# Kernel optimization log

Measured on AMD Instinct MI355X. Metric: run time of the kernel, lower is better.

The kernel has to match this reference:

```python
import jax, jax.numpy as jnp
import numpy as np

B, CIN, COUT = 4, 256, 256
H, W = 48, 48
KH = KW = 7
SH = SW = 1
PH = PW = 3
REL = COUT // 2  # rel_size with groups=1


def setup_inputs() -> dict:
    key = jax.random.key(0)
    ks = jax.random.split(key, 7)
    fan = float(CIN)
    x = jax.random.normal(ks[0], (B, CIN, H, W), jnp.float32)
    w_q = jax.random.normal(ks[1], (COUT, CIN), jnp.float32) * (2.0 / fan) ** 0.5
    w_k = jax.random.normal(ks[2], (COUT, CIN), jnp.float32) * (2.0 / fan) ** 0.5
    w_v = jax.random.normal(ks[3], (COUT, CIN), jnp.float32) * (2.0 / fan) ** 0.5
    bound = 1.0 / np.sqrt(COUT)
    bias = jax.random.uniform(ks[4], (1, COUT, 1, 1), jnp.float32, -bound, bound)
    rel_x = jax.random.normal(ks[5], (REL, KW), jnp.float32)
    rel_y = jax.random.normal(ks[6], (COUT - REL, KH), jnp.float32)
    return {"x": x, "w_q": w_q, "w_k": w_k, "w_v": w_v, "bias": bias,
            "rel_x": rel_x, "rel_y": rel_y}


def reference(x, w_q, w_k, w_v, bias, rel_x, rel_y):
    b = x.shape[0]
    ph, pw = H + 2 * PH, W + 2 * PW
    fh = (ph - KH) // SH + 1
    fw = (pw - KW) // SW + 1
    xp = jnp.pad(x, ((0, 0), (0, 0), (PH, PH), (PW, PW)))
    # 1x1 convs (groups=1) as channel matmuls
    vq = jnp.einsum('oc,bchw->bohw', w_q, xp)
    vk = jnp.einsum('oc,bchw->bohw', w_k, xp)
    vv = jnp.einsum('oc,bchw->bohw', w_v, xp)
    # query at window centers: [b, C, fh, fw]
    win_q = vq[:, :, (KH - 1) // 2: ph - KH // 2: SH, (KW - 1) // 2: pw - KW // 2: SW]
    # relative position terms (sum over channel halves)
    qx = jnp.einsum('bxhw,xk->bhwk', win_q[:, :REL], rel_x)        # [b,fh,fw,kw]
    qy = jnp.einsum('byhw,yk->bhwk', win_q[:, REL:], rel_y)        # [b,fh,fw,kh]
    # overlapping windows via gather (equivalent to torch unfold)
    I = jnp.arange(fh)[:, None] * SH + jnp.arange(KH)[None, :]     # [fh,kh]
    J = jnp.arange(fw)[:, None] * SW + jnp.arange(KW)[None, :]     # [fw,kw]
    win_k = vk[:, :, I[:, None, :, None], J[None, :, None, :]]     # [b,C,fh,fw,kh,kw]
    # channel-summed attention logits (shared across channels, as in source)
    scores = jnp.einsum('bchw,bchwkl->bhwkl', win_q, win_k)
    scores = scores + qy[:, :, :, :, None] + qx[:, :, :, None, :]
    attn = jax.nn.softmax(scores.reshape(b, fh, fw, KH * KW), axis=-1)
    attn = attn.reshape(b, fh, fw, KH, KW)
    win_v = vv[:, :, I[:, None, :, None], J[None, :, None, :]]     # [b,C,fh,fw,kh,kw]
    out = jnp.einsum('bhwkl,bchwkl->bchw', attn, win_v) + bias
    return out
```

## Files before the change

### kernel.cpp

```cpp
#include <hip/hip_runtime.h>

#define BB 4
#define CC 256
#define HH 48
#define WW 48
#define HWHW 2304
#define KK 49
#define RELN 128

#define QSZ (BB*CC*HWHW)
#define ATTNOFF (3*QSZ)
#define SBUF_FLOATS (BB*HH*64*WW)
#define WTOFF (ATTNOFF + SBUF_FLOATS)
#define WT_FLOATS 196608
#define KBOFF (WTOFF + WT_FLOATS)
#define KB_FLOATS 3145728
#define RBOFF (KBOFF + KB_FLOATS)

typedef short bf16x8 __attribute__((ext_vector_type(8)));
typedef float f32x4 __attribute__((ext_vector_type(4)));

__device__ __forceinline__ void split_bf16(float f, unsigned short& hi, unsigned short& lo)
{
    unsigned u = __float_as_uint(f);
    hi = (unsigned short)(u >> 16);
    float r = f - __uint_as_float(u & 0xFFFF0000u);
    unsigned v = __float_as_uint(r);
    v += 0x7FFFu + ((v >> 16) & 1u);
    lo = (unsigned short)(v >> 16);
}

__device__ __forceinline__ void gload16(const uint4* g, uint4* l)
{
    __builtin_amdgcn_global_load_lds(
        (const __attribute__((address_space(1))) void*)g,
        (__attribute__((address_space(3))) void*)l, 16, 0, 0);
}

__global__ __launch_bounds__(256) void prep_kernel(
    const float* __restrict__ x,
    const float* __restrict__ wq, const float* __restrict__ wk,
    const float* __restrict__ wvp,
    const float* __restrict__ relx, const float* __restrict__ rely,
    unsigned short* __restrict__ xt, unsigned short* __restrict__ wt,
    float* __restrict__ ws)
{
    __shared__ unsigned short lds[32*520];
    const int bid = blockIdx.x;
    const int t = threadIdx.x;

    if (bid < 288) {
        const int b = bid / 72;
        const int hw0 = (bid % 72) * 32;
        const int hw = t & 31, cp = t >> 5;
        #pragma unroll 4
        for (int i = 0; i < 32; ++i) {
            int c = i*8 + cp;
            float f = x[((size_t)b*CC + c)*HWHW + hw0 + hw];
            unsigned short hi, lo; split_bf16(f, hi, lo);
            int ch = i*2;
            lds[hw*520 + ((ch       ^ (hw&7))*8) + cp] = hi;
            lds[hw*520 + (((ch + 1) ^ (hw&7))*8) + cp] = lo;
        }
        __syncthreads();
        const int hw2 = t >> 3, u = t & 7;
        uint4* xt4 = (uint4*)xt;
        const size_t rowbase = ((size_t)b*HWHW + hw0 + hw2) * 64;
        #pragma unroll
        for (int j = 0; j < 8; ++j) {
            int chunk = j*8 + u;
            uint4 v = *(const uint4*)&lds[hw2*520 + chunk*8];
            xt4[rowbase + chunk] = v;
        }
        return;
    }
    if (bid < 384) {
        const int tt = (bid - 288)*256 + t;
        const int m = tt >> 5, kg = tt & 31;
        const float* src = (m < 256) ? wq : (m < 512) ? wk : wvp;
        const float* row = src + (size_t)(m & 255)*256 + kg*8;
        unsigned short h[8], l[8];
        #pragma unroll
        for (int j = 0; j < 8; ++j) split_bf16(row[j], h[j], l[j]);
        uint4 hv, lv;
        hv.x = (unsigned)h[0] | ((unsigned)h[1]<<16); hv.y = (unsigned)h[2] | ((unsigned)h[3]<<16);
        hv.z = (unsigned)h[4] | ((unsigned)h[5]<<16); hv.w = (unsigned)h[6] | ((unsigned)h[7]<<16);
        lv.x = (unsigned)l[0] | ((unsigned)l[1]<<16); lv.y = (unsigned)l[2] | ((unsigned)l[3]<<16);
        lv.z = (unsigned)l[4] | ((unsigned)l[5]<<16); lv.w = (unsigned)l[6] | ((unsigned)l[7]<<16);
        uint4* dstrow = (uint4*)wt + (size_t)m*64;
        const int ks = kg >> 2, s_hi = 2*(kg & 3);
        dstrow[ks*8 + ( s_hi      ^ (m&7))] = hv;
        dstrow[ks*8 + ((s_hi + 1) ^ (m&7))] = lv;
        return;
    }
    if (bid < 576) {
        uint4* kb4 = (uint4*)(ws + KBOFF);
        const uint4 z = make_uint4(0u,0u,0u,0u);
        int u0 = (bid - 384)*256 + t;
        #pragma unroll
        for (int it = 0; it < 4; ++it) {
            int u = u0 + it*49152;
            int bch = u >> 7, rem = u & 127;
            int r16 = rem >> 3, gr = rem & 7;
            int r = (r16 < 3) ? r16 : 48 + r16;
            kb4[((size_t)bch*64 + r)*8 + gr] = z;
        }
        return;
    }
    {
        unsigned short* rb = (unsigned short*)(ws + RBOFF);
        #pragma unroll
        for (int it = 0; it < 4; ++it) {
            int idx = t + it*256;
            int gi  = idx & 7;
            int l   = (idx >> 3) & 15;
            int ck4 = (idx >> 7) & 3;
            int rel = idx >> 9;
            int isLo = gi >> 2, g4i = gi & 3;
            unsigned short vals[8];
            #pragma unroll
            for (int j = 0; j < 8; ++j) {
                int cl = ck4*32 + g4i*8 + j;
                float f = (l < 7) ? (rel ? rely[cl*7 + l] : relx[cl*7 + l]) : 0.f;
                unsigned short hi, lo; split_bf16(f, hi, lo);
                vals[j] = isLo ? lo : hi;
            }
            int slot = gi ^ (l & 7);
            unsigned short* dst = rb + (((size_t)rel*4 + ck4)*16 + l)*64 + slot*8;
            uint4 pack;
            pack.x = (unsigned)vals[0] | ((unsigned)vals[1]<<16);
            pack.y = (unsigned)vals[2] | ((unsigned)vals[3]<<16);
            pack.z = (unsigned)vals[4] | ((unsigned)vals[5]<<16);
            pack.w = (unsigned)vals[6] | ((unsigned)vals[7]<<16);
            *(uint4*)dst = pack;
        }
    }
}

__global__ __launch_bounds__(256) void proj_gemm_kernel(
    const unsigned short* __restrict__ xt,
    const unsigned short* __restrict__ wt,
    float* __restrict__ ws)
{
    __shared__ uint4 smem[2][1024];
    const int n0 = blockIdx.x * 64;
    const int m0 = blockIdx.y * 64;
    const int b = n0 / HWHW;
    const int hwb = n0 % HWHW;
    const int tid = threadIdx.x;
    const int wid = tid >> 6, ln = tid & 63;
    const int wm = wid >> 1, wn = wid & 1;
    const int l15 = ln & 15, g = ln >> 4;

    f32x4 acc[2][2];
    #pragma unroll
    for (int i = 0; i < 2; ++i)
        #pragma unroll
        for (int j = 0; j < 2; ++j) acc[i][j] = (f32x4){0.f,0.f,0.f,0.f};

    const uint4* wt4 = (const uint4*)wt;
    const uint4* xt4 = (const uint4*)xt;
    const int lrow = ln >> 3, lslot = ln & 7;

    #define STAGE(bf, ks)                                                          \
        {                                                                          \
            _Pragma("unroll")                                                      \
            for (int i = 0; i < 2; ++i) {                                          \
                int seg = wid*2 + i;                                               \
                int row = seg*8 + lrow;                                            \
                gload16(wt4 + (size_t)(m0 + row)*64 + (ks)*8 + lslot,              \
                        &smem[bf][seg*64]);                                        \
                gload16(xt4 + (size_t)(n0 + row)*64 + (ks)*8 + lslot,              \
                        &smem[bf][512 + seg*64]);                                  \
            }                                                                      \
        }

    STAGE(0, 0);
    #pragma unroll
    for (int ks = 0; ks < 8; ++ks) {
        const int cur = ks & 1;
        if (ks < 7) STAGE(cur ^ 1, ks + 1);
        if (ks < 7) asm volatile("s_waitcnt vmcnt(4)" ::: "memory");
        else        asm volatile("s_waitcnt vmcnt(0)" ::: "memory");
        __builtin_amdgcn_s_barrier();
        __builtin_amdgcn_sched_barrier(0);
        bf16x8 aH[2], aL[2], bH[2], bL[2];
        #pragma unroll
        for (int mt = 0; mt < 2; ++mt) {
            int rA = wm*32 + mt*16 + l15;
            aH[mt] = *(const bf16x8*)&smem[cur][rA*8 + ((2*g)   ^ (rA&7))];
            aL[mt] = *(const bf16x8*)&smem[cur][rA*8 + ((2*g+1) ^ (rA&7))];
        }
        #pragma unroll
        for (int nt = 0; nt < 2; ++nt) {
            int rB = wn*32 + nt*16 + l15;
            bH[nt] = *(const bf16x8*)&smem[cur][512 + rB*8 + ((2*g)   ^ (rB&7))];
            bL[nt] = *(const bf16x8*)&smem[cur][512 + rB*8 + ((2*g+1) ^ (rB&7))];
        }
        #pragma unroll
        for (int mt = 0; mt < 2; ++mt)
            #pragma unroll
            for (int nt = 0; nt < 2; ++nt) {
                acc[mt][nt] = __builtin_amdgcn_mfma_f32_16x16x32_bf16(aH[mt], bH[nt], acc[mt][nt], 0, 0, 0);
                acc[mt][nt] = __builtin_amdgcn_mfma_f32_16x16x32_bf16(aH[mt], bL[nt], acc[mt][nt], 0, 0, 0);
                acc[mt][nt] = __builtin_amdgcn_mfma_f32_16x16x32_bf16(aL[mt], bH[nt], acc[mt][nt], 0, 0, 0);
            }
        if (ks < 7) {
            asm volatile("s_waitcnt lgkmcnt(0)" ::: "memory");
            __builtin_amdgcn_s_barrier();
        }
    }
    #undef STAGE

    const int proj = m0 >> 8;
    if (proj == 2) {
        #pragma unroll
        for (int mt = 0; mt < 2; ++mt) {
            int chb = (m0 & 255) + wm*32 + mt*16 + 4*g;
            int ch4 = chb >> 2;
            #pragma unroll
            for (int nt = 0; nt < 2; ++nt) {
                int hw = hwb + wn*32 + nt*16 + l15;
                float* dst = ws + (size_t)2*QSZ + (((size_t)b*64 + ch4)*HWHW + hw)*4;
                *(f32x4*)dst = acc[mt][nt];
            }
        }
        return;
    }
    __syncthreads();
    unsigned short* eb = (unsigned short*)&smem[0][0];
    #pragma unroll
    for (int mt = 0; mt < 2; ++mt) {
        const int chb = (m0 & 255) + wm*32 + mt*16 + 4*g;
        const int ckl = (chb >> 5) & 1;
        const int p = chb & 31, g8 = p >> 3, half = (p >> 2) & 1;
        #pragma unroll
        for (int nt = 0; nt < 2; ++nt) {
            const int hwl = wn*32 + nt*16 + l15;
            const int w = (hwb + hwl) % 48;
            const int key = (proj == 0 ? w : w + 3) & 7;
            f32x4 v = acc[mt][nt];
            unsigned short h0,h1,h2,h3,q0,q1,q2,q3;
            split_bf16(v[0],h0,q0); split_bf16(v[1],h1,q1);
            split_bf16(v[2],h2,q2); split_bf16(v[3],h3,q3);
            uint2 hv, lv;
            hv.x = (unsigned)h0 | ((unsigned)h1<<16); hv.y = (unsigned)h2 | ((unsigned)h3<<16);
            lv.x = (unsigned)q0 | ((unsigned)q1<<16); lv.y = (unsigned)q2 | ((unsigned)q3<<16);
            const int base = (ckl*64 + hwl)*64;
            *(uint2*)(eb + base + ((g8 ^ key)*8 + half*4))     = hv;
            *(uint2*)(eb + base + (((g8+4) ^ key)*8 + half*4)) = lv;
        }
    }
    __syncthreads();
    const int ck0 = (m0 & 255) >> 5;
    if (proj == 0) {
        const uint4* src = (const uint4*)eb;
        uint4* qb4 = (uint4*)ws;
        #pragma unroll
        for (int ckl2 = 0; ckl2 < 2; ++ckl2) {
            uint4* dst = qb4 + (((size_t)b*8 + ck0 + ckl2)*HWHW + hwb)*8;
            #pragma unroll
            for (int it = 0; it < 2; ++it)
                dst[tid + it*256] = src[ckl2*512 + tid + it*256];
        }
    } else {
        uint4* kb4 = (uint4*)(ws + KBOFF);
        const uint4* src = (const uint4*)eb;
        #pragma unroll
        for (int it = 0; it < 4; ++it) {
            int u = tid + it*256;
            int row = u >> 3, gr = u & 7;
            int ckl2 = row >> 6, hwl2 = row & 63;
            int hw2 = hwb + hwl2, h2 = hw2/48, w2 = hw2%48;
            uint4* dst = kb4 + ((((size_t)b*8 + ck0 + ckl2)*48 + h2)*64 + (w2+3))*8;
            dst[gr] = src[u];
        }
    }
}

__global__ __launch_bounds__(512) void scores2_kernel(float* __restrict__ ws)
{
    __shared__ unsigned short sAll[4096*8];
    __shared__ float sc[63][48];

    unsigned short* sQ = sAll;
    unsigned short* sK = sAll + 384*8;
    unsigned short* sR = sAll + 3968*8;

    const int bid = blockIdx.x;
    const int b = bid / 48, h = bid % 48;
    const int tid = threadIdx.x;
    const int wv = tid >> 6, ln = tid & 63;
    const int l15 = ln & 15, g4 = ln >> 4;
    const int key = l15 & 7;

    const unsigned short* QB = (const unsigned short*)ws;
    const unsigned short* KB = (const unsigned short*)(ws + KBOFF);
    const unsigned short* RB = (const unsigned short*)(ws + RBOFF);

    for (int u = tid; u < 63*48; u += 512) ((float*)sc)[u] = 0.f;

    const int dk = wv;
    const int hp = h + dk - 3;
    const bool dok = (wv < 7) && (hp >= 0) && (hp < 48);

    f32x4 acc[6], qx[3], qy[3];
    #pragma unroll
    for (int i = 0; i < 6; ++i) acc[i] = (f32x4){0.f,0.f,0.f,0.f};
    #pragma unroll
    for (int i = 0; i < 3; ++i) { qx[i] = (f32x4){0.f,0.f,0.f,0.f}; qy[i] = (f32x4){0.f,0.f,0.f,0.f}; }

    for (int ck = 0; ck < 8; ++ck) {
        #pragma unroll
        for (int e = 0; e < 8; ++e) {
            const int I = wv*8 + e;
            uint4* dst = (uint4*)sAll + I*64;
            if (I < 6) {
                int unit = I*64 + ln; int row = unit >> 3, gr = unit & 7;
                const uint4* src = (const uint4*)QB
                    + ((((size_t)b*8 + ck)*48 + h)*48 + row)*8 + gr;
                gload16(src, dst);
            } else if (I < 62) {
                int uk = (I-6)*64 + ln;
                int kri = uk >> 9;
                int wi = uk & 511; int row = wi >> 3, gr = wi & 7;
                int kh = h + kri - 3;
                if (kh >= 0 && kh < 48) {
                    const uint4* src = (const uint4*)KB
                        + ((((size_t)b*8 + ck)*48 + kh)*64 + row)*8 + gr;
                    gload16(src, dst);
                }
            } else {
                int ur = (I-62)*64 + ln; int row = ur >> 3, gr = ur & 7;
                int rel = ck >> 2, c4 = ck & 3;
                const uint4* src = (const uint4*)RB
                    + (((size_t)rel*4 + c4)*16 + row)*8 + gr;
                gload16(src, dst);
            }
        }
        __syncthreads();

        bf16x8 AH[3], AL[3];
        #pragma unroll
        for (int i = 0; i < 3; ++i) {
            const unsigned short* qr = sQ + (16*i + l15)*64;
            AH[i] = *(const bf16x8*)(qr + ((g4       ^ key)*8));
            AL[i] = *(const bf16x8*)(qr + (((g4 + 4) ^ key)*8));
        }

        if (wv < 7) {
            if (dok) {
                const unsigned short* kbase = sK + dk*4096;
                bf16x8 BH[4], BL[4];
                #pragma unroll
                for (int j = 0; j < 4; ++j) {
                    const unsigned short* kr = kbase + (j*16 + l15)*64;
                    BH[j] = *(const bf16x8*)(kr + ((g4       ^ key)*8));
                    BL[j] = *(const bf16x8*)(kr + (((g4 + 4) ^ key)*8));
                }
                #pragma unroll
                for (int i = 0; i < 3; ++i) {
                    acc[i*2]   = __builtin_amdgcn_mfma_f32_16x16x32_bf16(AH[i], BH[i],   acc[i*2],   0,0,0);
                    acc[i*2]   = __builtin_amdgcn_mfma_f32_16x16x32_bf16(AH[i], BL[i],   acc[i*2],   0,0,0);
                    acc[i*2]   = __builtin_amdgcn_mfma_f32_16x16x32_bf16(AL[i], BH[i],   acc[i*2],   0,0,0);
                    acc[i*2+1] = __builtin_amdgcn_mfma_f32_16x16x32_bf16(AH[i], BH[i+1], acc[i*2+1], 0,0,0);
                    acc[i*2+1] = __builtin_amdgcn_mfma_f32_16x16x32_bf16(AH[i], BL[i+1], acc[i*2+1], 0,0,0);
                    acc[i*2+1] = __builtin_amdgcn_mfma_f32_16x16x32_bf16(AL[i], BH[i+1], acc[i*2+1], 0,0,0);
                }
            }
        } else {
            const unsigned short* rr = sR + l15*64;
            bf16x8 RH = *(const bf16x8*)(rr + ((g4       ^ key)*8));
            bf16x8 RL = *(const bf16x8*)(rr + (((g4 + 4) ^ key)*8));
            if (ck < 4) {
                #pragma unroll
                for (int i = 0; i < 3; ++i) {
                    qx[i] = __builtin_amdgcn_mfma_f32_16x16x32_bf16(AH[i], RH, qx[i], 0,0,0);
                    qx[i] = __builtin_amdgcn_mfma_f32_16x16x32_bf16(AH[i], RL, qx[i], 0,0,0);
                    qx[i] = __builtin_amdgcn_mfma_f32_16x16x32_bf16(AL[i], RH, qx[i], 0,0,0);
                }
            } else {
                #pragma unroll
                for (int i = 0; i < 3; ++i) {
                    qy[i] = __builtin_amdgcn_mfma_f32_16x16x32_bf16(AH[i], RH, qy[i], 0,0,0);
                    qy[i] = __builtin_amdgcn_mfma_f32_16x16x32_bf16(AH[i], RL, qy[i], 0,0,0);
                    qy[i] = __builtin_amdgcn_mfma_f32_16x16x32_bf16(AL[i], RH, qy[i], 0,0,0);
                }
            }
        }
        __syncthreads();
    }

    const int n = l15;
    if (wv < 7) {
        if (dok) {
            #pragma unroll
            for (int i = 0; i < 3; ++i)
                #pragma unroll
                for (int a = 0; a < 2; ++a) {
                    f32x4 A = acc[i*2+a];
                    #pragma unroll
                    for (int r = 0; r < 4; ++r) {
                        int m = 4*g4 + r;
                        int dl = n - m + a*16;
                        if (dl >= 0 && dl < 7)
                            sc[dk*7 + dl][16*i + m] = A[r];
                    }
                }
        }
    } else {
        if (n < 7) {
            #pragma unroll
            for (int i = 0; i < 3; ++i)
                #pragma unroll
                for (int r = 0; r < 4; ++r) {
                    sc[49 + n][16*i + 4*g4 + r] = qx[i][r];
                    sc[56 + n][16*i + 4*g4 + r] = qy[i][r];
                }
        }
    }
    __syncthreads();

    if (tid < 48) {
        const int w = tid;
        float tot[KK], rx[7], ry[7];
        #pragma unroll
        for (int i = 0; i < KK; ++i) tot[i] = sc[i][w];
        #pragma unroll
        for (int l = 0; l < 7; ++l) { rx[l] = sc[49+l][w]; ry[l] = sc[56+l][w]; }
        float mx = -1e30f;
        #pragma unroll
        for (int dk2 = 0; dk2 < 7; ++dk2)
            #pragma unroll
            for (int dl = 0; dl < 7; ++dl) {
                tot[dk2*7+dl] += ry[dk2] + rx[dl];
                mx = fmaxf(mx, tot[dk2*7+dl]);
            }
        float sum = 0.f;
        #pragma unroll
        for (int i = 0; i < KK; ++i) { float e = __expf(tot[i]-mx); tot[i]=e; sum += e; }
        float inv = 1.f/sum;
        float* base = ws + ATTNOFF + ((size_t)(b*HH + h)*64)*WW + w;
        #pragma unroll
        for (int i = 0; i < KK; ++i) base[(size_t)i*WW] = tot[i]*inv;
    }
}

__global__ __launch_bounds__(128) void pv_kernel(
    const float* __restrict__ bias,
    const float* __restrict__ ws,
    float* __restrict__ out)
{
    const float* vbuf = ws + (size_t)2*QSZ;
    const float* attn = ws + ATTNOFF;

    const int bid = blockIdx.x;
    const int pxt = bid % 18;
    const int pgq = (bid / 18) % 16;
    const int b   = bid / (18*16);

    const int tid = threadIdx.x;
    const int pxg = tid & 31;
    const int pg  = pgq*4 + (tid >> 5);

    const int hw0 = pxt*128 + pxg*4;
    const int w0 = hw0 % WW;
    const int h0 = hw0 / WW;

    const float* vb = vbuf + ((size_t)b*64 + pg)*HWHW*4;
    const float* ab = attn + ((size_t)(b*HH + h0)*64)*WW;

    const float4 b4 = *(const float4*)(bias + pg*4);
    f32x4 bias4 = (f32x4){b4.x, b4.y, b4.z, b4.w};
    f32x4 acc[4];
    #pragma unroll
    for (int p = 0; p < 4; ++p) acc[p] = bias4;

    #pragma unroll
    for (int dk = 0; dk < 7; ++dk) {
        const int gr = h0 + dk - 3;
        const bool rok = (gr >= 0 && gr < HH);
        f32x4 vrow[10];
        #pragma unroll
        for (int jj = 0; jj < 10; ++jj) {
            const int gc = w0 - 3 + jj;
            vrow[jj] = (rok && gc >= 0 && gc < WW)
                ? *(const f32x4*)(vb + ((size_t)gr*WW + gc)*4)
                : (f32x4){0.f,0.f,0.f,0.f};
        }
        const float* arow = ab + (size_t)(dk*7)*WW + w0;
        #pragma unroll
        for (int dl = 0; dl < 7; ++dl) {
            const float4 av = *(const float4*)(arow + (size_t)dl*WW);
            acc[0] += vrow[dl+0] * av.x;
            acc[1] += vrow[dl+1] * av.y;
            acc[2] += vrow[dl+2] * av.z;
            acc[3] += vrow[dl+3] * av.w;
        }
    }
    #pragma unroll
    for (int c = 0; c < 4; ++c) {
        float4 o;
        o.x = acc[0][c]; o.y = acc[1][c]; o.z = acc[2][c]; o.w = acc[3][c];
        *(float4*)(out + ((size_t)b*CC + pg*4 + c)*HWHW + hw0) = o;
    }
}

extern "C" void kernel_launch(void* const* d_in, const int* in_sizes, int n_in,
                              void* d_out, int out_size, void* d_ws, size_t ws_size,
                              hipStream_t stream) {
    const float* x    = (const float*)d_in[0];
    const float* wq   = (const float*)d_in[1];
    const float* wk   = (const float*)d_in[2];
    const float* wv   = (const float*)d_in[3];
    const float* bias = (const float*)d_in[4];
    const float* relx = (const float*)d_in[5];
    const float* rely = (const float*)d_in[6];
    float* ws  = (float*)d_ws;
    float* out = (float*)d_out;
    unsigned short* xt = (unsigned short*)d_out;
    unsigned short* wt = (unsigned short*)(ws + WTOFF);

    prep_kernel<<<dim3(577), dim3(256), 0, stream>>>(x, wq, wk, wv, relx, rely, xt, wt, ws);
    proj_gemm_kernel<<<dim3(144, 12), dim3(256), 0, stream>>>(xt, wt, ws);
    scores2_kernel<<<dim3(BB*HH), dim3(512), 0, stream>>>(ws);
    pv_kernel<<<dim3(BB*16*18), dim3(128), 0, stream>>>(bias, ws, out);
}
```

Measured before the change: 74.91 us.

## Split scores kernel over channel chunks and add a separate reduce-softmax kernel

The scores kernel now splits the 8 channel chunks across 4 blocks per (batch,row), so the grid grows from 192 to 768 blocks. Each block writes its partial score and relative-position sums to workspace. A new reduce_softmax kernel adds the four partials and runs the softmax. The aim is to fill more of the 256 CUs, at the cost of one extra launch, extra global traffic for the partials, and the Q tile being reloaded in every split.

```diff
diff --git a/kernel.cpp b/kernel.cpp
--- a/kernel.cpp
+++ b/kernel.cpp
@@ -16,6 +16,7 @@
 #define KBOFF (WTOFF + WT_FLOATS)
 #define KB_FLOATS 3145728
 #define RBOFF (KBOFF + KB_FLOATS)
+#define PARTOFF (RBOFF + 4096)
 
 typedef short bf16x8 __attribute__((ext_vector_type(8)));
 typedef float f32x4 __attribute__((ext_vector_type(4)));
@@ -288,7 +289,9 @@
     unsigned short* sR = sAll + 3968*8;
 
     const int bid = blockIdx.x;
-    const int b = bid / 48, h = bid % 48;
+    const int ckp = bid & 3;
+    const int h = (bid >> 2) % 48;
+    const int b = bid / 192;
     const int tid = threadIdx.x;
     const int wv = tid >> 6, ln = tid & 63;
     const int l15 = ln & 15, g4 = ln >> 4;
@@ -310,7 +313,8 @@
     #pragma unroll
     for (int i = 0; i < 3; ++i) { qx[i] = (f32x4){0.f,0.f,0.f,0.f}; qy[i] = (f32x4){0.f,0.f,0.f,0.f}; }
 
-    for (int ck = 0; ck < 8; ++ck) {
+    for (int cki = 0; cki < 2; ++cki) {
+        const int ck = ckp*2 + cki;
         #pragma unroll
         for (int e = 0; e < 8; ++e) {
             const int I = wv*8 + e;
@@ -421,13 +425,33 @@
     }
     __syncthreads();
 
-    if (tid < 48) {
-        const int w = tid;
+    float* pdst = ws + PARTOFF + ((size_t)(b*HH + h)*4 + ckp)*3024;
+    for (int u = tid; u < 3024; u += 512) pdst[u] = ((const float*)sc)[u];
+}
+
+__global__ __launch_bounds__(256) void reduce_softmax_kernel(float* __restrict__ ws)
+{
+    __shared__ float red[63][48];
+    const int bh = blockIdx.x;
+    const int t = threadIdx.x;
+    const float* pb = ws + PARTOFF + (size_t)bh*4*3024;
+
+    for (int u = t; u < 756; u += 256) {
+        f32x4 a = *(const f32x4*)(pb + u*4)
+                + *(const f32x4*)(pb + 3024 + u*4)
+                + *(const f32x4*)(pb + 2*3024 + u*4)
+                + *(const f32x4*)(pb + 3*3024 + u*4);
+        *(f32x4*)&((float*)red)[u*4] = a;
+    }
+    __syncthreads();
+
+    if (t < WW) {
+        const int w = t;
         float tot[KK], rx[7], ry[7];
         #pragma unroll
-        for (int i = 0; i < KK; ++i) tot[i] = sc[i][w];
-        #pragma unroll
-        for (int l = 0; l < 7; ++l) { rx[l] = sc[49+l][w]; ry[l] = sc[56+l][w]; }
+        for (int i = 0; i < KK; ++i) tot[i] = red[i][w];
+        #pragma unroll
+        for (int l = 0; l < 7; ++l) { rx[l] = red[49+l][w]; ry[l] = red[56+l][w]; }
         float mx = -1e30f;
         #pragma unroll
         for (int dk2 = 0; dk2 < 7; ++dk2)
@@ -440,7 +464,7 @@
         #pragma unroll
         for (int i = 0; i < KK; ++i) { float e = __expf(tot[i]-mx); tot[i]=e; sum += e; }
         float inv = 1.f/sum;
-        float* base = ws + ATTNOFF + ((size_t)(b*HH + h)*64)*WW + w;
+        float* base = ws + ATTNOFF + (size_t)bh*64*WW + w;
         #pragma unroll
         for (int i = 0; i < KK; ++i) base[(size_t)i*WW] = tot[i]*inv;
     }
@@ -523,6 +547,7 @@
 
     prep_kernel<<<dim3(577), dim3(256), 0, stream>>>(x, wq, wk, wv, relx, rely, xt, wt, ws);
     proj_gemm_kernel<<<dim3(144, 12), dim3(256), 0, stream>>>(xt, wt, ws);
-    scores2_kernel<<<dim3(BB*HH), dim3(512), 0, stream>>>(ws);
+    scores2_kernel<<<dim3(BB*HH*4), dim3(512), 0, stream>>>(ws);
+    reduce_softmax_kernel<<<dim3(BB*HH), dim3(256), 0, stream>>>(ws);
     pv_kernel<<<dim3(BB*16*18), dim3(128), 0, stream>>>(bias, ws, out);
 }
```

Result: no change. 75.29 us (+0.5%).

## Double-buffer LDS staging in scores2 kernel to overlap loads with MFMA

Applied to the files above, without the earlier changes.

Splits the shared staging buffer into two halves and prefetches chunk ck+1 with direct-to-LDS loads while chunk ck is being computed, using vmcnt-based waits and raw barriers instead of __syncthreads. K-row indices are clamped rather than skipped, so every lane issues a fixed number of loads and the vmcnt counts stay predictable. This is meant to hide global-load latency behind the MFMA work. In exchange, LDS use doubles (two 64KB buffers plus the score tile), which may limit how many blocks fit per CU, and out-of-range K rows are now loaded redundantly.

```diff
diff --git a/kernel.cpp b/kernel.cpp
--- a/kernel.cpp
+++ b/kernel.cpp
@@ -280,12 +280,8 @@
 
 __global__ __launch_bounds__(512) void scores2_kernel(float* __restrict__ ws)
 {
-    __shared__ unsigned short sAll[4096*8];
+    __shared__ unsigned short sAll[2][4096*8];
     __shared__ float sc[63][48];
-
-    unsigned short* sQ = sAll;
-    unsigned short* sK = sAll + 384*8;
-    unsigned short* sR = sAll + 3968*8;
 
     const int bid = blockIdx.x;
     const int b = bid / 48, h = bid % 48;
@@ -310,35 +306,45 @@
     #pragma unroll
     for (int i = 0; i < 3; ++i) { qx[i] = (f32x4){0.f,0.f,0.f,0.f}; qy[i] = (f32x4){0.f,0.f,0.f,0.f}; }
 
+    #define SSTAGE(bf, ck)                                                         \
+        {                                                                          \
+            _Pragma("unroll")                                                      \
+            for (int e = 0; e < 8; ++e) {                                          \
+                const int I = wv*8 + e;                                            \
+                uint4* dst = (uint4*)sAll[bf] + I*64;                              \
+                if (I < 6) {                                                       \
+                    int unit = I*64 + ln; int row = unit >> 3, gr = unit & 7;      \
+                    gload16((const uint4*)QB                                       \
+                        + ((((size_t)b*8 + (ck))*48 + h)*48 + row)*8 + gr, dst);   \
+                } else if (I < 62) {                                               \
+                    int uk = (I-6)*64 + ln;                                        \
+                    int kri = uk >> 9;                                             \
+                    int wi = uk & 511; int row = wi >> 3, gr = wi & 7;             \
+                    int kh = h + kri - 3;                                          \
+                    int khc = kh < 0 ? 0 : (kh > 47 ? 47 : kh);                    \
+                    gload16((const uint4*)KB                                       \
+                        + ((((size_t)b*8 + (ck))*48 + khc)*64 + row)*8 + gr, dst); \
+                } else {                                                           \
+                    int ur = (I-62)*64 + ln; int row = ur >> 3, gr = ur & 7;       \
+                    int rel = (ck) >> 2, c4 = (ck) & 3;                            \
+                    gload16((const uint4*)RB                                       \
+                        + (((size_t)rel*4 + c4)*16 + row)*8 + gr, dst);            \
+                }                                                                  \
+            }                                                                      \
+        }
+
+    SSTAGE(0, 0);
     for (int ck = 0; ck < 8; ++ck) {
-        #pragma unroll
-        for (int e = 0; e < 8; ++e) {
-            const int I = wv*8 + e;
-            uint4* dst = (uint4*)sAll + I*64;
-            if (I < 6) {
-                int unit = I*64 + ln; int row = unit >> 3, gr = unit & 7;
-                const uint4* src = (const uint4*)QB
-                    + ((((size_t)b*8 + ck)*48 + h)*48 + row)*8 + gr;
-                gload16(src, dst);
-            } else if (I < 62) {
-                int uk = (I-6)*64 + ln;
-                int kri = uk >> 9;
-                int wi = uk & 511; int row = wi >> 3, gr = wi & 7;
-                int kh = h + kri - 3;
-                if (kh >= 0 && kh < 48) {
-                    const uint4* src = (const uint4*)KB
-                        + ((((size_t)b*8 + ck)*48 + kh)*64 + row)*8 + gr;
-                    gload16(src, dst);
-                }
-            } else {
-                int ur = (I-62)*64 + ln; int row = ur >> 3, gr = ur & 7;
-                int rel = ck >> 2, c4 = ck & 3;
-                const uint4* src = (const uint4*)RB
-                    + (((size_t)rel*4 + c4)*16 + row)*8 + gr;
-                gload16(src, dst);
-            }
-        }
-        __syncthreads();
+        const int cur = ck & 1;
+        if (ck < 7) SSTAGE(cur ^ 1, ck + 1);
+        if (ck < 7) asm volatile("s_waitcnt vmcnt(8)" ::: "memory");
+        else        asm volatile("s_waitcnt vmcnt(0)" ::: "memory");
+        __builtin_amdgcn_s_barrier();
+        __builtin_amdgcn_sched_barrier(0);
+
+        const unsigned short* sQ = sAll[cur];
+        const unsigned short* sK = sAll[cur] + 384*8;
+        const unsigned short* sR = sAll[cur] + 3968*8;
 
         bf16x8 AH[3], AL[3];
         #pragma unroll
@@ -388,8 +394,12 @@
                 }
             }
         }
-        __syncthreads();
-    }
+        if (ck < 7) {
+            asm volatile("s_waitcnt lgkmcnt(0)" ::: "memory");
+            __builtin_amdgcn_s_barrier();
+        }
+    }
+    #undef SSTAGE
 
     const int n = l15;
     if (wv < 7) {
```

Result: faster. 72.44 us (-3.3%).
